# Kernel optimization log

Measured on AMD Instinct MI355X. Metric: run time of the kernel, lower is better.

The kernel has to match this reference:

```python
import jax, jax.numpy as jnp
import numpy as np

SIGMA = 0.1
B = 1.0
SPATIAL_WEIGHT = 0.5
EPS = 1e-5


def setup_inputs() -> dict:
    key = jax.random.key(0)
    k1, k2 = jax.random.split(key)
    N, C, H, W = 2, 256, 64, 64
    I_features = jax.random.normal(k1, (N, C, H, W), dtype=jnp.float32)
    T_features = jax.random.normal(k2, (N, C, H, W), dtype=jnp.float32)
    return {"I_features": I_features, "T_features": T_features}


def _calc_cx(raw):
    # raw: [N, P_T, H, W]; min + exp-softmax over the target-patch axis (axis=1)
    mn = jnp.min(raw, axis=1, keepdims=True)
    rel = raw / (mn + EPS)
    w = jnp.exp((B - rel) / SIGMA)
    return w / jnp.sum(w, axis=1, keepdims=True)


def reference(I_features, T_features):
    N, C, H, W = I_features.shape
    P = H * W

    # ---- spatial branch: L2 distances on a normalized meshgrid (C=2) ----
    rows = jnp.arange(H, dtype=jnp.float32) / (H + 1)
    cols = jnp.arange(W, dtype=jnp.float32) / (W + 1)
    grid = jnp.stack(jnp.meshgrid(rows, cols, indexing="ij"))  # [2, H, W]
    g = grid.reshape(2, P)                                      # [2, P]
    sq = jnp.sum(g * g, axis=0)                                 # [P]
    d = sq[:, None] + sq[None, :] - 2.0 * (g.T @ g)             # [P_I, P_T]
    d = jnp.clip(d, 0.0)
    raw_sp = d.T.reshape(1, P, H, W)  # [1, P_T, H, W]; identical per sample
    cx_sp = _calc_cx(raw_sp)

    # ---- feature branch: cosine similarity via centered, L2-normed feats ----
    meanT = jnp.mean(T_features, axis=(0, 2, 3), keepdims=True)
    Ic = I_features - meanT
    Tc = T_features - meanT
    In = Ic / jnp.linalg.norm(Ic, axis=1, keepdims=True)
    Tn = Tc / jnp.linalg.norm(Tc, axis=1, keepdims=True)
    Iv = In.reshape(N, C, P)
    Tv = Tn.reshape(N, C, P)
    dot = jnp.einsum("ncq,ncp->nqp", Tv, Iv)  # [N, P_T, P_I]
    raw_feat = ((1.0 - dot) / 2.0).reshape(N, P, H, W)
    cx_feat = _calc_cx(raw_feat)

    # ---- combine, max over I positions, mean over T patches, -log, mean ----
    cx = (1.0 - SPATIAL_WEIGHT) * cx_feat + SPATIAL_WEIGHT * cx_sp  # [N,P,H,W]
    m = jnp.max(cx, axis=(2, 3))  # [N, P]
    m = jnp.mean(m, axis=1)       # [N]
    return jnp.mean(-jnp.log(m))
```

## Files before the change

kernel.cpp:

```cpp
#include <hip/hip_runtime.h>
#include <math.h>

#define PP 4096
#define CC 256
#define NN 2

typedef __attribute__((ext_vector_type(8))) short short8;
typedef __attribute__((ext_vector_type(4))) float f32x4;

__device__ __forceinline__ short f2bf(float x) {
    union { float f; unsigned u; } un; un.f = x;
    unsigned r = un.u + 0x7fffu + ((un.u >> 16) & 1u);
    return (short)(r >> 16);
}

__device__ __forceinline__ void gld_lds16(const short* g, short* l) {
    __builtin_amdgcn_global_load_lds(
        (const __attribute__((address_space(1))) unsigned int*)g,
        (__attribute__((address_space(3))) unsigned int*)l, 16, 0, 0);
}

__global__ __launch_bounds__(256) void mean_kernel(const float* __restrict__ T,
                                                   float* __restrict__ meanT,
                                                   unsigned* __restrict__ mn_enc,
                                                   float* __restrict__ S,
                                                   float* __restrict__ diagw) {
    int c = blockIdx.x, tid = threadIdx.x;
    float s = 0.f;
    for (int n = 0; n < NN; n++)
        for (int p = tid; p < PP; p += 256)
            s += T[(size_t)(n * CC + c) * PP + p];
    __shared__ float red[256];
    red[tid] = s; __syncthreads();
    for (int st = 128; st > 0; st >>= 1) {
        if (tid < st) red[tid] += red[tid + st];
        __syncthreads();
    }
    if (tid == 0) meanT[c] = red[0] * (1.0f / (NN * PP));
    int base = blockIdx.x * 32;
    if (tid < 32) {
        mn_enc[base + tid] = 0xFFFFFFFFu;
        S[base + tid] = 0.f;
        diagw[base + tid] = 0.f;
    }
}

__global__ __launch_bounds__(256) void normalize_kernel(const float* __restrict__ I,
                                                        const float* __restrict__ T,
                                                        const float* __restrict__ meanT,
                                                        short* __restrict__ InT,
                                                        short* __restrict__ TnT) {
    int pc = blockIdx.x * 32;
    int n = blockIdx.y;
    int which = blockIdx.z;
    const float* X = which ? T : I;
    short* Y = which ? TnT : InT;

    __shared__ float tile[CC][33];
    __shared__ float red[8][32];
    __shared__ float invn[32];

    int tid = threadIdx.x;
    int pl = tid & 31, c0 = tid >> 5;
    float sq = 0.f;
    for (int c = c0; c < CC; c += 8) {
        float v = X[(size_t)(n * CC + c) * PP + pc + pl] - meanT[c];
        tile[c][pl] = v;
        sq += v * v;
    }
    red[c0][pl] = sq;
    __syncthreads();
    if (tid < 32) {
        float s = 0.f;
        for (int k = 0; k < 8; k++) s += red[k][tid];
        invn[tid] = 1.0f / sqrtf(s);
    }
    __syncthreads();
    for (int rr = 0; rr < 32; rr += 2) {
        int r = rr + (tid >> 7);
        int c2 = (tid & 127) * 2;
        float v0 = tile[c2][r] * invn[r];
        float v1 = tile[c2 + 1][r] * invn[r];
        unsigned pack = ((unsigned)(unsigned short)f2bf(v1) << 16) |
                        (unsigned)(unsigned short)f2bf(v0);
        *(unsigned*)&Y[(size_t)(n * PP + pc + r) * CC + c2] = pack;
    }
}

template <int MODE>
__global__ __launch_bounds__(512, 6) void cx_gemm(const short* __restrict__ TnT,
                                                  const short* __restrict__ InT,
                                                  unsigned* __restrict__ mn_enc,
                                                  float* __restrict__ S,
                                                  float* __restrict__ diagw) {
    const int n = blockIdx.z;
    const short* __restrict__ A = TnT + (size_t)n * PP * CC;
    const short* __restrict__ B = InT + (size_t)n * PP * CC;
    const int q0 = blockIdx.y * 128, p0 = blockIdx.x * 128;

    __shared__ __align__(16) short As[128 * 64];
    __shared__ __align__(16) short Bs[128 * 64];
    __shared__ float red[8][64];

    const int tid = threadIdx.x;
    const int l = tid & 63, wv = tid >> 6;
    const int lm = l & 15, quad = l >> 4;
    const int wr = (wv & 3) * 32, wc = (wv >> 2) * 64;

    const int srow = tid >> 3;
    const int gk = ((tid & 7) ^ (srow & 7)) * 8;
    const short* Ag = A + (size_t)(q0 + srow) * CC + gk;
    const short* Bg = B + (size_t)(p0 + srow) * CC + gk;
    short* Al = As + tid * 8;
    short* Bl = Bs + tid * 8;

    f32x4 acc[2][4] = {};

    for (int k0 = 0; k0 < CC; k0 += 64) {
        __syncthreads();
        gld_lds16(Ag + k0, Al);
        gld_lds16(Ag + 64 * CC + k0, Al + 4096);
        gld_lds16(Bg + k0, Bl);
        gld_lds16(Bg + 64 * CC + k0, Bl + 4096);
        __syncthreads();

#pragma unroll
        for (int ksub = 0; ksub < 2; ksub++) {
            const int c = ksub * 4 + quad;
            short8 a[2], b[4];
#pragma unroll
            for (int i = 0; i < 2; i++)
                a[i] = *(const short8*)&As[(wr + i * 16 + lm) * 64 + (c ^ (lm & 7)) * 8];
#pragma unroll
            for (int j = 0; j < 4; j++)
                b[j] = *(const short8*)&Bs[(wc + j * 16 + lm) * 64 + (c ^ (lm & 7)) * 8];
#pragma unroll
            for (int i = 0; i < 2; i++)
#pragma unroll
                for (int j = 0; j < 4; j++)
                    acc[i][j] = __builtin_amdgcn_mfma_f32_16x16x32_bf16(a[i], b[j], acc[i][j], 0, 0, 0);
        }
    }

    if (MODE == 0) {
#pragma unroll
        for (int j = 0; j < 4; j++) {
            float m = 3.4e38f;
#pragma unroll
            for (int i = 0; i < 2; i++)
#pragma unroll
                for (int e = 0; e < 4; e++)
                    m = fminf(m, (1.0f - acc[i][j][e]) * 0.5f);
            m = fminf(m, __shfl_xor(m, 16));
            m = fminf(m, __shfl_xor(m, 32));
            if (quad == 0) red[wv][j * 16 + lm] = m;
        }
        __syncthreads();
        if (tid < 128) {
            int grp = tid >> 6, idx = tid & 63;
            float m = fminf(fminf(red[grp * 4 + 0][idx], red[grp * 4 + 1][idx]),
                            fminf(red[grp * 4 + 2][idx], red[grp * 4 + 3][idx]));
            unsigned u = __float_as_uint(m);
            u = (u & 0x80000000u) ? ~u : (u | 0x80000000u);
            atomicMin(&mn_enc[n * PP + p0 + tid], u);
        }
    } else {
#pragma unroll
        for (int j = 0; j < 4; j++) {
            const int col = p0 + wc + j * 16 + lm;
            unsigned e = mn_enc[n * PP + col];
            unsigned u = (e & 0x80000000u) ? (e & 0x7fffffffu) : ~e;
            float mnv = __uint_as_float(u);
            float inv2 = 14.4269504f / (mnv + 1e-5f);
            float s = 0.f;
#pragma unroll
            for (int i = 0; i < 2; i++)
#pragma unroll
                for (int e2 = 0; e2 < 4; e2++) {
                    float raw = (1.0f - acc[i][j][e2]) * 0.5f;
                    float w = exp2f(fmaf(raw, -inv2, 14.4269504f));
                    s += w;
                    int q = q0 + wr + i * 16 + quad * 4 + e2;
                    if (q == col) diagw[n * PP + q] = w;
                }
            s += __shfl_xor(s, 16);
            s += __shfl_xor(s, 32);
            if (quad == 0) red[wv][j * 16 + lm] = s;
        }
        __syncthreads();
        if (tid < 128) {
            int grp = tid >> 6, idx = tid & 63;
            float s = red[grp * 4 + 0][idx] + red[grp * 4 + 1][idx] +
                      red[grp * 4 + 2][idx] + red[grp * 4 + 3][idx];
            atomicAdd(&S[n * PP + p0 + tid], s);
        }
    }
}

__global__ __launch_bounds__(1024) void finalize_kernel(const float* __restrict__ S,
                                                        const float* __restrict__ diagw,
                                                        float* __restrict__ out) {
    __shared__ float red[1024];
    int tid = threadIdx.x;
    int n = tid >> 9, t = tid & 511;
    float s = 0.f;
    for (int i = t; i < PP; i += 512)
        s += diagw[n * PP + i] / S[n * PP + i];
    red[tid] = s; __syncthreads();
    for (int st = 256; st > 0; st >>= 1) {
        if (t < st) red[n * 512 + t] += red[n * 512 + t + st];
        __syncthreads();
    }
    if (tid == 0) {
        float m0 = 0.5f + 0.5f * (red[0] / (float)PP);
        float m1 = 0.5f + 0.5f * (red[512] / (float)PP);
        out[0] = 0.5f * (-logf(m0) - logf(m1));
    }
}

extern "C" void kernel_launch(void* const* d_in, const int* in_sizes, int n_in,
                              void* d_out, int out_size, void* d_ws, size_t ws_size,
                              hipStream_t stream) {
    const float* I = (const float*)d_in[0];
    const float* T = (const float*)d_in[1];
    float* out = (float*)d_out;

    char* ws = (char*)d_ws;
    const size_t SZ_BF = (size_t)NN * PP * CC * sizeof(short);
    short* InT = (short*)ws;
    short* TnT = (short*)(ws + SZ_BF);
    float* meanT = (float*)(ws + 2 * SZ_BF);
    unsigned* mn = (unsigned*)(ws + 2 * SZ_BF + 32768);
    float* S = (float*)(ws + 2 * SZ_BF + 2 * 32768);
    float* diagw = (float*)(ws + 2 * SZ_BF + 3 * 32768);

    mean_kernel<<<CC, 256, 0, stream>>>(T, meanT, mn, S, diagw);
    normalize_kernel<<<dim3(PP / 32, NN, 2), 256, 0, stream>>>(I, T, meanT, InT, TnT);
    cx_gemm<0><<<dim3(PP / 128, PP / 128, NN), 512, 0, stream>>>(TnT, InT, mn, S, diagw);
    cx_gemm<1><<<dim3(PP / 128, PP / 128, NN), 512, 0, stream>>>(TnT, InT, mn, S, diagw);
    finalize_kernel<<<1, 1024, 0, stream>>>(S, diagw, out);
}
```

Before: 130.6 us.

## Double-buffer GEMM K-loop with 32-wide stages and fold finalize into last block

The GEMM main loop moves from single-buffered 64-wide K tiles with two barriers per step to double-buffered 32-wide K tiles, prefetching the next slice into LDS while the current one feeds MFMAs, with a new XOR swizzle. Separately, the finalize kernel is removed: the last block of the MODE 1 GEMM, found through an atomic ticket counter, does the final reduction and log. This aims to hide global-to-LDS latency and save one kernel launch, at the cost of more loop iterations, a threadfence in every block and a serialized tail reduction.

```diff
diff --git a/kernel.cpp b/kernel.cpp
--- a/kernel.cpp
+++ b/kernel.cpp
@@ -24,7 +24,8 @@
                                                    float* __restrict__ meanT,
                                                    unsigned* __restrict__ mn_enc,
                                                    float* __restrict__ S,
-                                                   float* __restrict__ diagw) {
+                                                   float* __restrict__ diagw,
+                                                   unsigned* __restrict__ ticket) {
     int c = blockIdx.x, tid = threadIdx.x;
     float s = 0.f;
     for (int n = 0; n < NN; n++)
@@ -43,6 +44,7 @@
         S[base + tid] = 0.f;
         diagw[base + tid] = 0.f;
     }
+    if (blockIdx.x == 0 && tid == 64) ticket[0] = 0u;
 }
 
 __global__ __launch_bounds__(256) void normalize_kernel(const float* __restrict__ I,
@@ -92,14 +94,16 @@
                                                   const short* __restrict__ InT,
                                                   unsigned* __restrict__ mn_enc,
                                                   float* __restrict__ S,
-                                                  float* __restrict__ diagw) {
+                                                  float* __restrict__ diagw,
+                                                  unsigned* __restrict__ ticket,
+                                                  float* __restrict__ out) {
     const int n = blockIdx.z;
     const short* __restrict__ A = TnT + (size_t)n * PP * CC;
     const short* __restrict__ B = InT + (size_t)n * PP * CC;
     const int q0 = blockIdx.y * 128, p0 = blockIdx.x * 128;
 
-    __shared__ __align__(16) short As[128 * 64];
-    __shared__ __align__(16) short Bs[128 * 64];
+    __shared__ __align__(16) short As[2][128 * 32];
+    __shared__ __align__(16) short Bs[2][128 * 32];
     __shared__ float red[8][64];
 
     const int tid = threadIdx.x;
@@ -107,39 +111,38 @@
     const int lm = l & 15, quad = l >> 4;
     const int wr = (wv & 3) * 32, wc = (wv >> 2) * 64;
 
-    const int srow = tid >> 3;
-    const int gk = ((tid & 7) ^ (srow & 7)) * 8;
-    const short* Ag = A + (size_t)(q0 + srow) * CC + gk;
-    const short* Bg = B + (size_t)(p0 + srow) * CC + gk;
-    short* Al = As + tid * 8;
-    short* Bl = Bs + tid * 8;
+    const int srow = tid >> 2;
+    const int gchunk = (tid & 3) ^ (srow & 3) ^ ((srow >> 2) & 3);
+    const short* Ag = A + (size_t)(q0 + srow) * CC + gchunk * 8;
+    const short* Bg = B + (size_t)(p0 + srow) * CC + gchunk * 8;
+
+    const int rslot = (quad ^ (lm & 3) ^ (lm >> 2)) * 8;
 
     f32x4 acc[2][4] = {};
 
-    for (int k0 = 0; k0 < CC; k0 += 64) {
-        __syncthreads();
-        gld_lds16(Ag + k0, Al);
-        gld_lds16(Ag + 64 * CC + k0, Al + 4096);
-        gld_lds16(Bg + k0, Bl);
-        gld_lds16(Bg + 64 * CC + k0, Bl + 4096);
-        __syncthreads();
-
-#pragma unroll
-        for (int ksub = 0; ksub < 2; ksub++) {
-            const int c = ksub * 4 + quad;
-            short8 a[2], b[4];
-#pragma unroll
-            for (int i = 0; i < 2; i++)
-                a[i] = *(const short8*)&As[(wr + i * 16 + lm) * 64 + (c ^ (lm & 7)) * 8];
+    gld_lds16(Ag, &As[0][tid * 8]);
+    gld_lds16(Bg, &Bs[0][tid * 8]);
+
+    for (int it = 0; it < 8; it++) {
+        __syncthreads();
+        if (it < 7) {
+            gld_lds16(Ag + (it + 1) * 32, &As[(it + 1) & 1][tid * 8]);
+            gld_lds16(Bg + (it + 1) * 32, &Bs[(it + 1) & 1][tid * 8]);
+        }
+        const short* __restrict__ Asb = As[it & 1];
+        const short* __restrict__ Bsb = Bs[it & 1];
+        short8 a[2], b[4];
+#pragma unroll
+        for (int i = 0; i < 2; i++)
+            a[i] = *(const short8*)&Asb[(wr + i * 16 + lm) * 32 + rslot];
+#pragma unroll
+        for (int j = 0; j < 4; j++)
+            b[j] = *(const short8*)&Bsb[(wc + j * 16 + lm) * 32 + rslot];
+#pragma unroll
+        for (int i = 0; i < 2; i++)
 #pragma unroll
             for (int j = 0; j < 4; j++)
-                b[j] = *(const short8*)&Bs[(wc + j * 16 + lm) * 64 + (c ^ (lm & 7)) * 8];
-#pragma unroll
-            for (int i = 0; i < 2; i++)
-#pragma unroll
-                for (int j = 0; j < 4; j++)
-                    acc[i][j] = __builtin_amdgcn_mfma_f32_16x16x32_bf16(a[i], b[j], acc[i][j], 0, 0, 0);
-        }
+                acc[i][j] = __builtin_amdgcn_mfma_f32_16x16x32_bf16(a[i], b[j], acc[i][j], 0, 0, 0);
     }
 
     if (MODE == 0) {
@@ -194,27 +197,34 @@
                       red[grp * 4 + 2][idx] + red[grp * 4 + 3][idx];
             atomicAdd(&S[n * PP + p0 + tid], s);
         }
-    }
-}
-
-__global__ __launch_bounds__(1024) void finalize_kernel(const float* __restrict__ S,
-                                                        const float* __restrict__ diagw,
-                                                        float* __restrict__ out) {
-    __shared__ float red[1024];
-    int tid = threadIdx.x;
-    int n = tid >> 9, t = tid & 511;
-    float s = 0.f;
-    for (int i = t; i < PP; i += 512)
-        s += diagw[n * PP + i] / S[n * PP + i];
-    red[tid] = s; __syncthreads();
-    for (int st = 256; st > 0; st >>= 1) {
-        if (t < st) red[n * 512 + t] += red[n * 512 + t + st];
-        __syncthreads();
-    }
-    if (tid == 0) {
-        float m0 = 0.5f + 0.5f * (red[0] / (float)PP);
-        float m1 = 0.5f + 0.5f * (red[512] / (float)PP);
-        out[0] = 0.5f * (-logf(m0) - logf(m1));
+
+        __shared__ unsigned rank_s;
+        __threadfence();
+        __syncthreads();
+        if (tid == 0) rank_s = atomicAdd(ticket, 1u);
+        __syncthreads();
+        if (rank_s == 32 * 32 * NN - 1) {
+            __threadfence();
+            float s0 = 0.f, s1 = 0.f;
+            for (int i = tid; i < PP; i += 512) {
+                s0 += diagw[i] / S[i];
+                s1 += diagw[PP + i] / S[PP + i];
+            }
+#pragma unroll
+            for (int off = 32; off > 0; off >>= 1) {
+                s0 += __shfl_xor(s0, off);
+                s1 += __shfl_xor(s1, off);
+            }
+            if (l == 0) { red[0][wv] = s0; red[1][wv] = s1; }
+            __syncthreads();
+            if (tid == 0) {
+                float t0 = 0.f, t1 = 0.f;
+                for (int k = 0; k < 8; k++) { t0 += red[0][k]; t1 += red[1][k]; }
+                float m0 = 0.5f + 0.5f * (t0 / (float)PP);
+                float m1 = 0.5f + 0.5f * (t1 / (float)PP);
+                out[0] = -0.5f * (logf(m0) + logf(m1));
+            }
+        }
     }
 }
 
@@ -233,10 +243,10 @@
     unsigned* mn = (unsigned*)(ws + 2 * SZ_BF + 32768);
     float* S = (float*)(ws + 2 * SZ_BF + 2 * 32768);
     float* diagw = (float*)(ws + 2 * SZ_BF + 3 * 32768);
-
-    mean_kernel<<<CC, 256, 0, stream>>>(T, meanT, mn, S, diagw);
+    unsigned* ticket = (unsigned*)(ws + 2 * SZ_BF + 4 * 32768);
+
+    mean_kernel<<<CC, 256, 0, stream>>>(T, meanT, mn, S, diagw, ticket);
     normalize_kernel<<<dim3(PP / 32, NN, 2), 256, 0, stream>>>(I, T, meanT, InT, TnT);
-    cx_gemm<0><<<dim3(PP / 128, PP / 128, NN), 512, 0, stream>>>(TnT, InT, mn, S, diagw);
-    cx_gemm<1><<<dim3(PP / 128, PP / 128, NN), 512, 0, stream>>>(TnT, InT, mn, S, diagw);
-    finalize_kernel<<<1, 1024, 0, stream>>>(S, diagw, out);
-}
+    cx_gemm<0><<<dim3(PP / 128, PP / 128, NN), 512, 0, stream>>>(TnT, InT, mn, S, diagw, ticket, out);
+    cx_gemm<1><<<dim3(PP / 128, PP / 128, NN), 512, 0, stream>>>(TnT, InT, mn, S, diagw, ticket, out);
+}
```

Measured after the change: 382.8 us. 193% more time.
